# Optimization experiments

Measured on AMD Instinct MI355X. Metric: run time of the kernel, lower is better.

Reference implementation:

```python
import jax, jax.numpy as jnp
import numpy as np

N = 200000   # octree nodes at this depth (in_h == out_h for stride=1)
K = 27       # kdim = 3*3*3
C_IN = 32
C_OUT = 32


def setup_inputs() -> dict:
    key = jax.random.key(0)
    k1, k2, k3 = jax.random.split(key, 3)
    data = jax.random.normal(k1, (N, C_IN), dtype=jnp.float32)
    weights = jax.random.normal(k2, (K, C_IN, C_OUT), dtype=jnp.float32) * 0.05
    raw = jax.random.randint(k3, (N, K), 0, N + N // 10)
    neigh = jnp.where(raw < N, raw, -1).astype(jnp.int64)
    return {"data": data, "weights": weights, "neigh": neigh}


def reference(data, weights, neigh):
    # gather neighbor features, zero-filled where neigh == -1
    valid = neigh >= 0                                 # [N, K]
    safe_idx = jnp.where(valid, neigh, 0)
    gathered = jnp.where(valid[..., None], data[safe_idx], 0.0)  # [N, K, C_in]
    # buffered GEMM: out[n, o] = sum_{k, c} gathered[n, k, c] * weights[k, c, o]
    out = jnp.einsum('nkc,kco->no', gathered, weights)           # [N, C_out]
    return out
```

## Files before the change

kernel.cpp:

```cpp
#include <hip/hip_runtime.h>
#include <hip/hip_bf16.h>

#define N_NODES 200000
#define KDIM 27
#define C_IN 32
#define C_OUT 32

typedef __bf16 bf16x8 __attribute__((ext_vector_type(8)));
typedef float floatx4 __attribute__((ext_vector_type(4)));
typedef float float4_t __attribute__((ext_vector_type(4)));

__device__ inline bf16x8 zero_bf16x8() {
    bf16x8 z;
#pragma unroll
    for (int i = 0; i < 8; ++i) z[i] = (__bf16)0.0f;
    return z;
}

__global__ __launch_bounds__(256) void convert_data_kernel(
    const float* __restrict__ src, __bf16* __restrict__ dst) {
    int i = blockIdx.x * 256 + threadIdx.x;
    const float4_t* s = (const float4_t*)src;
    float4_t v0 = s[2 * i];
    float4_t v1 = s[2 * i + 1];
    bf16x8 o;
    o[0] = (__bf16)v0[0]; o[1] = (__bf16)v0[1];
    o[2] = (__bf16)v0[2]; o[3] = (__bf16)v0[3];
    o[4] = (__bf16)v1[0]; o[5] = (__bf16)v1[1];
    o[6] = (__bf16)v1[2]; o[7] = (__bf16)v1[3];
    ((bf16x8*)dst)[i] = o;
}

__global__ __launch_bounds__(256) void pack_weights_kernel(
    const float* __restrict__ w, __bf16* __restrict__ wp) {
    int id = blockIdx.x * 256 + threadIdx.x;
    int j = id & 7;
    int l = (id >> 3) & 63;
    int t = (id >> 9) & 1;
    int kk = id >> 10;
    int c = ((l >> 4) << 3) + j;
    int o = t * 16 + (l & 15);
    wp[id] = (__bf16)w[(kk * C_IN + c) * C_OUT + o];
}

__global__ __launch_bounds__(256) void octconv_main_kernel(
    const int* __restrict__ neigh, const __bf16* __restrict__ data_bf,
    const __bf16* __restrict__ wpack, float* __restrict__ out) {
    int tid  = threadIdx.x;
    int wave = tid >> 6;
    int lane = tid & 63;
    int node_base = (blockIdx.x * 4 + wave) * 32;
    int r16  = lane & 15;
    int half = lane >> 4;
    int cb   = half << 3;
    int m0   = node_base + r16;
    int m1   = m0 + 16;

    floatx4 acc00 = {0.f, 0.f, 0.f, 0.f};
    floatx4 acc01 = {0.f, 0.f, 0.f, 0.f};
    floatx4 acc10 = {0.f, 0.f, 0.f, 0.f};
    floatx4 acc11 = {0.f, 0.f, 0.f, 0.f};

    const bf16x8* wp = (const bf16x8*)wpack;

#pragma unroll 3
    for (int kk = 0; kk < KDIM; ++kk) {
        int idx0 = (m0 < N_NODES) ? neigh[m0 * KDIM + kk] : -1;
        int idx1 = (m1 < N_NODES) ? neigh[m1 * KDIM + kk] : -1;

        bf16x8 a0 = zero_bf16x8();
        bf16x8 a1 = zero_bf16x8();
        if (idx0 >= 0) a0 = *(const bf16x8*)(data_bf + ((size_t)idx0 << 5) + cb);
        if (idx1 >= 0) a1 = *(const bf16x8*)(data_bf + ((size_t)idx1 << 5) + cb);

        bf16x8 b0 = wp[(kk * 2 + 0) * 64 + lane];
        bf16x8 b1 = wp[(kk * 2 + 1) * 64 + lane];

        acc00 = __builtin_amdgcn_mfma_f32_16x16x32_bf16(a0, b0, acc00, 0, 0, 0);
        acc01 = __builtin_amdgcn_mfma_f32_16x16x32_bf16(a0, b1, acc01, 0, 0, 0);
        acc10 = __builtin_amdgcn_mfma_f32_16x16x32_bf16(a1, b0, acc10, 0, 0, 0);
        acc11 = __builtin_amdgcn_mfma_f32_16x16x32_bf16(a1, b1, acc11, 0, 0, 0);
    }

#pragma unroll
    for (int r = 0; r < 4; ++r) {
        int row = half * 4 + r;
        int n0 = node_base + row;
        int n1 = n0 + 16;
        if (n0 < N_NODES) {
            out[n0 * C_OUT + r16]      = acc00[r];
            out[n0 * C_OUT + 16 + r16] = acc01[r];
        }
        if (n1 < N_NODES) {
            out[n1 * C_OUT + r16]      = acc10[r];
            out[n1 * C_OUT + 16 + r16] = acc11[r];
        }
    }
}

extern "C" void kernel_launch(void* const* d_in, const int* in_sizes, int n_in,
                              void* d_out, int out_size, void* d_ws, size_t ws_size,
                              hipStream_t stream) {
    const float* data    = (const float*)d_in[0];
    const float* weights = (const float*)d_in[1];
    const int*   neigh   = (const int*)d_in[2];
    float*       out     = (float*)d_out;

    __bf16* data_bf = (__bf16*)d_ws;
    __bf16* wpack   = (__bf16*)((char*)d_ws + (size_t)N_NODES * C_IN * 2);

    hipLaunchKernelGGL(convert_data_kernel, dim3((N_NODES * C_IN / 8 + 255) / 256),
                       dim3(256), 0, stream, data, data_bf);
    hipLaunchKernelGGL(pack_weights_kernel, dim3((KDIM * C_IN * C_OUT + 255) / 256),
                       dim3(256), 0, stream, weights, wpack);
    int blocks = (N_NODES + 127) / 128;
    hipLaunchKernelGGL(octconv_main_kernel, dim3(blocks), dim3(256), 0, stream,
                       neigh, data_bf, wpack, out);
}
```

Before: 193.8 us.

## Software-pipeline neighbor gathers with register prefetch and zero-row sentinel

Restructures the main loop into a software pipeline. Neighbor indices are prefetched several steps ahead and gathered feature rows and weights a few steps ahead in register ring buffers. Invalid neighbors are clamped to an appended zero row instead of branching, and the loop is fully unrolled. Nontemporal loads and stores are used for streaming traffic. The aim is to hide gather latency behind MFMA work, at the cost of higher register pressure and possibly lower occupancy.

```diff
diff --git a/kernel.cpp b/kernel.cpp
--- a/kernel.cpp
+++ b/kernel.cpp
@@ -5,6 +5,10 @@
 #define KDIM 27
 #define C_IN 32
 #define C_OUT 32
+
+#define PF 4
+#define IPD 4
+#define IB (PF + IPD)
 
 typedef __bf16 bf16x8 __attribute__((ext_vector_type(8)));
 typedef float floatx4 __attribute__((ext_vector_type(4)));
@@ -21,14 +25,17 @@
     const float* __restrict__ src, __bf16* __restrict__ dst) {
     int i = blockIdx.x * 256 + threadIdx.x;
     const float4_t* s = (const float4_t*)src;
-    float4_t v0 = s[2 * i];
-    float4_t v1 = s[2 * i + 1];
+    float4_t v0 = __builtin_nontemporal_load(&s[2 * i]);
+    float4_t v1 = __builtin_nontemporal_load(&s[2 * i + 1]);
     bf16x8 o;
     o[0] = (__bf16)v0[0]; o[1] = (__bf16)v0[1];
     o[2] = (__bf16)v0[2]; o[3] = (__bf16)v0[3];
     o[4] = (__bf16)v1[0]; o[5] = (__bf16)v1[1];
     o[6] = (__bf16)v1[2]; o[7] = (__bf16)v1[3];
     ((bf16x8*)dst)[i] = o;
+    if (blockIdx.x == 0 && threadIdx.x < 4) {
+        ((bf16x8*)dst)[N_NODES * 4 + threadIdx.x] = zero_bf16x8();
+    }
 }
 
 __global__ __launch_bounds__(256) void pack_weights_kernel(
@@ -46,40 +53,66 @@
 __global__ __launch_bounds__(256) void octconv_main_kernel(
     const int* __restrict__ neigh, const __bf16* __restrict__ data_bf,
     const __bf16* __restrict__ wpack, float* __restrict__ out) {
-    int tid  = threadIdx.x;
-    int wave = tid >> 6;
-    int lane = tid & 63;
-    int node_base = (blockIdx.x * 4 + wave) * 32;
-    int r16  = lane & 15;
-    int half = lane >> 4;
-    int cb   = half << 3;
-    int m0   = node_base + r16;
-    int m1   = m0 + 16;
+    const int tid  = threadIdx.x;
+    const int wave = tid >> 6;
+    const int lane = tid & 63;
+    const int node_base = (blockIdx.x * 4 + wave) * 32;
+    const int r16  = lane & 15;
+    const int half = lane >> 4;
+    const int cb   = half << 3;
+    const int m0   = node_base + r16;
+    const int m1   = m0 + 16;
+    const int sm0 = (m0 < N_NODES) ? m0 : (N_NODES - 1);
+    const int sm1 = (m1 < N_NODES) ? m1 : (N_NODES - 1);
+    const int* __restrict__ nrow0 = neigh + sm0 * KDIM;
+    const int* __restrict__ nrow1 = neigh + sm1 * KDIM;
+    const __bf16* __restrict__ dch = data_bf + cb;
+    const bf16x8* __restrict__ wp  = (const bf16x8*)wpack;
 
     floatx4 acc00 = {0.f, 0.f, 0.f, 0.f};
     floatx4 acc01 = {0.f, 0.f, 0.f, 0.f};
     floatx4 acc10 = {0.f, 0.f, 0.f, 0.f};
     floatx4 acc11 = {0.f, 0.f, 0.f, 0.f};
 
-    const bf16x8* wp = (const bf16x8*)wpack;
+    int i0buf[IB], i1buf[IB];
+    bf16x8 a0b[PF], a1b[PF], b0b[PF], b1b[PF];
 
-#pragma unroll 3
+#pragma unroll
+    for (int t = 0; t < IB; ++t) {
+        i0buf[t] = __builtin_nontemporal_load(&nrow0[t]);
+        i1buf[t] = __builtin_nontemporal_load(&nrow1[t]);
+    }
+#pragma unroll
+    for (int t = 0; t < PF; ++t) {
+        unsigned u0 = (unsigned)i0buf[t]; if (u0 > (unsigned)N_NODES) u0 = N_NODES;
+        unsigned u1 = (unsigned)i1buf[t]; if (u1 > (unsigned)N_NODES) u1 = N_NODES;
+        a0b[t] = *(const bf16x8*)(dch + ((size_t)u0 << 5));
+        a1b[t] = *(const bf16x8*)(dch + ((size_t)u1 << 5));
+        b0b[t] = wp[(t * 2 + 0) * 64 + lane];
+        b1b[t] = wp[(t * 2 + 1) * 64 + lane];
+    }
+
+#pragma unroll
     for (int kk = 0; kk < KDIM; ++kk) {
-        int idx0 = (m0 < N_NODES) ? neigh[m0 * KDIM + kk] : -1;
-        int idx1 = (m1 < N_NODES) ? neigh[m1 * KDIM + kk] : -1;
+        const int s = kk % PF;
+        acc00 = __builtin_amdgcn_mfma_f32_16x16x32_bf16(a0b[s], b0b[s], acc00, 0, 0, 0);
+        acc01 = __builtin_amdgcn_mfma_f32_16x16x32_bf16(a0b[s], b1b[s], acc01, 0, 0, 0);
+        acc10 = __builtin_amdgcn_mfma_f32_16x16x32_bf16(a1b[s], b0b[s], acc10, 0, 0, 0);
+        acc11 = __builtin_amdgcn_mfma_f32_16x16x32_bf16(a1b[s], b1b[s], acc11, 0, 0, 0);
 
-        bf16x8 a0 = zero_bf16x8();
-        bf16x8 a1 = zero_bf16x8();
-        if (idx0 >= 0) a0 = *(const bf16x8*)(data_bf + ((size_t)idx0 << 5) + cb);
-        if (idx1 >= 0) a1 = *(const bf16x8*)(data_bf + ((size_t)idx1 << 5) + cb);
-
-        bf16x8 b0 = wp[(kk * 2 + 0) * 64 + lane];
-        bf16x8 b1 = wp[(kk * 2 + 1) * 64 + lane];
-
-        acc00 = __builtin_amdgcn_mfma_f32_16x16x32_bf16(a0, b0, acc00, 0, 0, 0);
-        acc01 = __builtin_amdgcn_mfma_f32_16x16x32_bf16(a0, b1, acc01, 0, 0, 0);
-        acc10 = __builtin_amdgcn_mfma_f32_16x16x32_bf16(a1, b0, acc10, 0, 0, 0);
-        acc11 = __builtin_amdgcn_mfma_f32_16x16x32_bf16(a1, b1, acc11, 0, 0, 0);
+        if (kk + PF < KDIM) {
+            const int t = kk + PF;
+            unsigned u0 = (unsigned)i0buf[t % IB]; if (u0 > (unsigned)N_NODES) u0 = N_NODES;
+            unsigned u1 = (unsigned)i1buf[t % IB]; if (u1 > (unsigned)N_NODES) u1 = N_NODES;
+            a0b[s] = *(const bf16x8*)(dch + ((size_t)u0 << 5));
+            a1b[s] = *(const bf16x8*)(dch + ((size_t)u1 << 5));
+            b0b[s] = wp[(t * 2 + 0) * 64 + lane];
+            b1b[s] = wp[(t * 2 + 1) * 64 + lane];
+        }
+        if (kk + IB < KDIM) {
+            i0buf[kk % IB] = __builtin_nontemporal_load(&nrow0[kk + IB]);
+            i1buf[kk % IB] = __builtin_nontemporal_load(&nrow1[kk + IB]);
+        }
     }
 
 #pragma unroll
@@ -88,12 +121,12 @@
         int n0 = node_base + row;
         int n1 = n0 + 16;
         if (n0 < N_NODES) {
-            out[n0 * C_OUT + r16]      = acc00[r];
-            out[n0 * C_OUT + 16 + r16] = acc01[r];
+            __builtin_nontemporal_store(acc00[r], &out[n0 * C_OUT + r16]);
+            __builtin_nontemporal_store(acc01[r], &out[n0 * C_OUT + 16 + r16]);
         }
         if (n1 < N_NODES) {
-            out[n1 * C_OUT + r16]      = acc10[r];
-            out[n1 * C_OUT + 16 + r16] = acc11[r];
+            __builtin_nontemporal_store(acc10[r], &out[n1 * C_OUT + r16]);
+            __builtin_nontemporal_store(acc11[r], &out[n1 * C_OUT + 16 + r16]);
         }
     }
 }
@@ -107,7 +140,7 @@
     float*       out     = (float*)d_out;
 
     __bf16* data_bf = (__bf16*)d_ws;
-    __bf16* wpack   = (__bf16*)((char*)d_ws + (size_t)N_NODES * C_IN * 2);
+    __bf16* wpack   = (__bf16*)((char*)d_ws + (size_t)(N_NODES + 1) * C_IN * sizeof(__bf16));
 
     hipLaunchKernelGGL(convert_data_kernel, dim3((N_NODES * C_IN / 8 + 255) / 256),
                        dim3(256), 0, stream, data, data_bf);
```

Measured after the change: 177.3 us. -8.5%, faster.
